# Kernel optimization log

Measured on AMD Instinct MI355X. Metric: run time of the kernel, lower is better.

Reference implementation:

```python
import jax, jax.numpy as jnp
import numpy as np

B, T, IN, H, FC, OUT = 512, 1024, 64, 128, 128, 1


def _glorot(key, shape, fan):
    bound = 1.0 / np.sqrt(fan)
    return jax.random.uniform(key, shape, jnp.float32, -bound, bound)


def setup_inputs() -> dict:
    key = jax.random.key(0)
    ks = jax.random.split(key, 16)
    inp = {"x": jax.random.normal(ks[0], (B, T, IN), jnp.float32)}
    # GRU layer 0 (input IN -> H), layer 1 (H -> H). PyTorch layout: [3H, in], [3H, H]
    inp["W_ih0"] = _glorot(ks[1], (3 * H, IN), H)
    inp["W_hh0"] = _glorot(ks[2], (3 * H, H), H)
    inp["b_ih0"] = _glorot(ks[3], (3 * H,), H)
    inp["b_hh0"] = _glorot(ks[4], (3 * H,), H)
    inp["W_ih1"] = _glorot(ks[5], (3 * H, H), H)
    inp["W_hh1"] = _glorot(ks[6], (3 * H, H), H)
    inp["b_ih1"] = _glorot(ks[7], (3 * H,), H)
    inp["b_hh1"] = _glorot(ks[8], (3 * H,), H)
    inp["fc1_w"] = _glorot(ks[9], (FC, H), H)
    inp["fc1_b"] = _glorot(ks[10], (FC,), H)
    inp["fc2_w"] = _glorot(ks[11], (OUT, FC), FC)
    inp["fc2_b"] = _glorot(ks[12], (OUT,), FC)
    return inp


def _gru_layer(x_seq, W_ih, W_hh, b_ih, b_hh):
    # x_seq: [T, B, in]. Precompute all input projections in one big GEMM.
    xg = jnp.einsum("tbi,gi->tbg", x_seq, W_ih) + b_ih  # [T, B, 3H]
    h0 = jnp.zeros((x_seq.shape[1], W_hh.shape[1]), x_seq.dtype)

    def step(h, xg_t):
        hg = h @ W_hh.T + b_hh  # [B, 3H]
        xr, xz, xn = jnp.split(xg_t, 3, axis=-1)
        hr, hz, hn = jnp.split(hg, 3, axis=-1)
        r = jax.nn.sigmoid(xr + hr)
        z = jax.nn.sigmoid(xz + hz)
        n = jnp.tanh(xn + r * hn)
        h_new = (1.0 - z) * n + z * h
        return h_new, h_new

    _, hs = jax.lax.scan(step, h0, xg)
    return hs  # [T, B, H]


def reference(x, W_ih0, W_hh0, b_ih0, b_hh0, W_ih1, W_hh1, b_ih1, b_hh1,
              fc1_w, fc1_b, fc2_w, fc2_b):
    xs = jnp.transpose(x, (1, 0, 2))  # [T, B, IN]
    h1 = _gru_layer(xs, W_ih0, W_hh0, b_ih0, b_hh0)  # dropout inactive (eval)
    h2 = _gru_layer(h1, W_ih1, W_hh1, b_ih1, b_hh1)
    last = h2[-1]  # [B, H] == gru_out[:, -1, :]
    y = jax.nn.relu(last @ fc1_w.T + fc1_b)
    return y @ fc2_w.T + fc2_b  # [B, OUT]
```

## Files before the change

### kernel.cpp

```cpp
#include <hip/hip_runtime.h>
#include <hip/hip_fp16.h>
#include <stdint.h>

#define TT   1024
#define NIN  64
#define HH   128
#define GG   384
#define RPB  2
#define NWG  256
#define NTHR 768

#define WB_IH0 0
#define WB_HH0 3072
#define WB_IH1 9216
#define WB_HH1 15360

typedef _Float16 half2v __attribute__((ext_vector_type(2)));

__device__ __forceinline__ float fdot2(uint32_t a, uint32_t b, float c) {
    return __builtin_amdgcn_fdot2(__builtin_bit_cast(half2v, a),
                                  __builtin_bit_cast(half2v, b), c, false);
}
__device__ __forceinline__ uint32_t pack2f(float a, float b) {
    half2v v; v[0] = (_Float16)a; v[1] = (_Float16)b;
    return __builtin_bit_cast(uint32_t, v);
}
__device__ __forceinline__ float sigm(float v)     { return 1.f / (1.f + __expf(-v)); }
__device__ __forceinline__ float tanhfast(float v) { return 2.f / (1.f + __expf(-2.f * v)) - 1.f; }

#define D4(A_, W_, S_) A_ = fdot2(W_.x, S_.x, A_); A_ = fdot2(W_.y, S_.y, A_); \
                       A_ = fdot2(W_.z, S_.z, A_); A_ = fdot2(W_.w, S_.w, A_);

#define PK8(M_, g_) M_(g_,0) M_(g_,1) M_(g_,2) M_(g_,3) M_(g_,4) M_(g_,5) M_(g_,6) M_(g_,7)
#define R8X(M_)     M_(0) M_(1) M_(2) M_(3) M_(4) M_(5) M_(6) M_(7)
#define DWDEF(g_,k_) uint4 W##g_##_##k_;
#define LW(g_,k_)    W##g_##_##k_ = wp[(g_)*wst + (k_)];
#define DG(g_,k_) D4(a##g_##_0, W##g_##_##k_, s0_) D4(a##g_##_1, W##g_##_##k_, s1_)
#define SK4(k_) { uint4 s0_ = pb0[k_], s1_ = pb1[k_]; DG(0,k_) DG(1,k_) DG(2,k_) DG(3,k_) }
#define SK3(k_) { uint4 s0_ = pb0[k_], s1_ = pb1[k_]; DG(0,k_) DG(1,k_) DG(2,k_) }

__global__ __launch_bounds__(256) void pack_weights(
    const float* __restrict__ Wih0, const float* __restrict__ Whh0,
    const float* __restrict__ Wih1, const float* __restrict__ Whh1,
    uint32_t* __restrict__ ws)
{
    const int i = blockIdx.x * 256 + threadIdx.x;
    const int P0 = 384 * 64 / 2, P1 = 384 * 128 / 2;
    const float* src; int off;
    if (i < P0)               { src = Wih0; off = i; }
    else if (i < P0 + P1)     { src = Whh0; off = i - P0; }
    else if (i < P0 + 2 * P1) { src = Wih1; off = i - P0 - P1; }
    else                      { src = Whh1; off = i - P0 - 2 * P1; }
    const float2 v = *(const float2*)(src + 2 * off);
    ws[i] = pack2f(v.x, v.y);
}

__global__ __launch_bounds__(NTHR)
__attribute__((amdgpu_waves_per_eu(3, 3)))
void gru_fused(
    const float* __restrict__ x,
    const uint32_t* __restrict__ wsw,
    const float* __restrict__ bih0, const float* __restrict__ bhh0,
    const float* __restrict__ bih1, const float* __restrict__ bhh1,
    const float* __restrict__ fc1w, const float* __restrict__ fc1b,
    const float* __restrict__ fc2w, const float* __restrict__ fc2b,
    float* __restrict__ out)
{
    __shared__ __align__(16) uint32_t xh[2][RPB][NIN / 2];
    __shared__ __align__(16) uint32_t h0h[RPB][HH / 2];
    __shared__ __align__(16) uint32_t h1h[RPB][HH / 2];
    __shared__ float h0f[RPB][HH];
    __shared__ float h1f[RPB][HH];
    __shared__ float pX0[RPB][GG];
    __shared__ __align__(16) float pH0q[RPB][96][2][4];
    __shared__ __align__(16) float pX1q[RPB][96][2][4];
    __shared__ __align__(16) float pH1q[RPB][96][2][4];

    const int lid  = threadIdx.x;
    const int row0 = blockIdx.x * RPB;

    PK8(DWDEF,0) PK8(DWDEF,1) PK8(DWDEF,2) PK8(DWDEF,3)
    float b0 = 0.f, b1 = 0.f, b2 = 0.f, b3 = 0.f;
    int gq_ = 0, kh_ = 0;
    const uint4 *pbA0 = nullptr, *pbA1 = nullptr;
    float2 xr2 = {0.f, 0.f};

    const uint4* wv = (const uint4*)wsw;

    if (lid < 128) {
        const int t = lid;
        const uint4* wp = wv + WB_IH0 + (3 * t) * 8; const int wst = 8;
        PK8(LW,0) PK8(LW,1) PK8(LW,2)
        b0 = bih0[3 * t]; b1 = bih0[3 * t + 1]; b2 = bih0[3 * t + 2];
    } else if (lid < 320) {
        const int t = lid - 128; gq_ = t >> 1; kh_ = t & 1;
        const uint4* wp = wv + WB_HH0 + (4 * gq_) * 16 + kh_ * 8; const int wst = 16;
        PK8(LW,0) PK8(LW,1) PK8(LW,2) PK8(LW,3)
        if (!kh_) { b0 = bhh0[4*gq_]; b1 = bhh0[4*gq_+1]; b2 = bhh0[4*gq_+2]; b3 = bhh0[4*gq_+3]; }
        pbA0 = (const uint4*)&h0h[0][0] + kh_ * 8;
        pbA1 = (const uint4*)&h0h[1][0] + kh_ * 8;
    } else if (lid < 512) {
        const int t = lid - 320; gq_ = t >> 1; kh_ = t & 1;
        const uint4* wp = wv + WB_IH1 + (4 * gq_) * 16 + kh_ * 8; const int wst = 16;
        PK8(LW,0) PK8(LW,1) PK8(LW,2) PK8(LW,3)
        if (!kh_) { b0 = bih1[4*gq_]; b1 = bih1[4*gq_+1]; b2 = bih1[4*gq_+2]; b3 = bih1[4*gq_+3]; }
        pbA0 = (const uint4*)&h0h[0][0] + kh_ * 8;
        pbA1 = (const uint4*)&h0h[1][0] + kh_ * 8;
    } else if (lid < 704) {
        const int t = lid - 512; gq_ = t >> 1; kh_ = t & 1;
        const uint4* wp = wv + WB_HH1 + (4 * gq_) * 16 + kh_ * 8; const int wst = 16;
        PK8(LW,0) PK8(LW,1) PK8(LW,2) PK8(LW,3)
        if (!kh_) { b0 = bhh1[4*gq_]; b1 = bhh1[4*gq_+1]; b2 = bhh1[4*gq_+2]; b3 = bhh1[4*gq_+3]; }
        pbA0 = (const uint4*)&h1h[0][0] + kh_ * 8;
        pbA1 = (const uint4*)&h1h[1][0] + kh_ * 8;
    } else {
        const int idx = lid - 704, r = idx >> 5, c = idx & 31;
        const float* xp = x + (size_t)(row0 + r) * TT * NIN + 2 * c;
        xh[0][r][c] = pack2f(xp[0], xp[1]);
        xr2 = *(const float2*)(xp + NIN);
    }

    if (lid < 128) {
        int r = lid >> 6, c = lid & 63;
        h0h[r][c] = 0u; h1h[r][c] = 0u;
    }
    if (lid < 256) {
        int r = lid >> 7, j = lid & 127;
        h0f[r][j] = 0.f; h1f[r][j] = 0.f;
    }
    __syncthreads();

    for (int i = 0; i <= TT; ++i) {
        if (lid < 128) {
            if (i < TT) {
                const uint4* pb0 = (const uint4*)&xh[i & 1][0][0];
                const uint4* pb1 = (const uint4*)&xh[i & 1][1][0];
                float a0_0 = b0, a0_1 = b0, a1_0 = b1, a1_1 = b1, a2_0 = b2, a2_1 = b2;
                R8X(SK3)
                const int g0 = 3 * lid;
                pX0[0][g0] = a0_0; pX0[0][g0+1] = a1_0; pX0[0][g0+2] = a2_0;
                pX0[1][g0] = a0_1; pX0[1][g0+1] = a1_1; pX0[1][g0+2] = a2_1;
            }
        } else if (lid < 320) {
            if (i < TT) {
                const uint4 *pb0 = pbA0, *pb1 = pbA1;
                float a0_0=b0,a0_1=b0,a1_0=b1,a1_1=b1,a2_0=b2,a2_1=b2,a3_0=b3,a3_1=b3;
                R8X(SK4)
                float4 v0 = {a0_0, a1_0, a2_0, a3_0};
                float4 v1 = {a0_1, a1_1, a2_1, a3_1};
                *(float4*)&pH0q[0][gq_][kh_][0] = v0;
                *(float4*)&pH0q[1][gq_][kh_][0] = v1;
            }
        } else if (lid < 512) {
            if (i >= 1) {
                const uint4 *pb0 = pbA0, *pb1 = pbA1;
                float a0_0=b0,a0_1=b0,a1_0=b1,a1_1=b1,a2_0=b2,a2_1=b2,a3_0=b3,a3_1=b3;
                R8X(SK4)
                float4 v0 = {a0_0, a1_0, a2_0, a3_0};
                float4 v1 = {a0_1, a1_1, a2_1, a3_1};
                *(float4*)&pX1q[0][gq_][kh_][0] = v0;
                *(float4*)&pX1q[1][gq_][kh_][0] = v1;
            }
        } else if (lid < 704) {
            if (i >= 1) {
                const uint4 *pb0 = pbA0, *pb1 = pbA1;
                float a0_0=b0,a0_1=b0,a1_0=b1,a1_1=b1,a2_0=b2,a2_1=b2,a3_0=b3,a3_1=b3;
                R8X(SK4)
                float4 v0 = {a0_0, a1_0, a2_0, a3_0};
                float4 v1 = {a0_1, a1_1, a2_1, a3_1};
                *(float4*)&pH1q[0][gq_][kh_][0] = v0;
                *(float4*)&pH1q[1][gq_][kh_][0] = v1;
            }
        } else {
            const int idx = lid - 704, r = idx >> 5, c = idx & 31;
            if (i + 1 < TT) xh[(i + 1) & 1][r][c] = pack2f(xr2.x, xr2.y);
            if (i + 2 < TT)
                xr2 = *(const float2*)(x + (size_t)(row0 + r) * TT * NIN
                                         + (size_t)(i + 2) * NIN + 2 * c);
        }
        __syncthreads();

        if (lid < 256) {
            if (i < TT) {
                const int r = lid >> 7, j = lid & 127;
                const int q = j >> 2, m = j & 3;
                float xr_ = pX0[r][j], xz_ = pX0[r][HH + j], xn_ = pX0[r][2*HH + j];
                float hr_ = pH0q[r][q][0][m]      + pH0q[r][q][1][m];
                float hz_ = pH0q[r][32 + q][0][m] + pH0q[r][32 + q][1][m];
                float hn_ = pH0q[r][64 + q][0][m] + pH0q[r][64 + q][1][m];
                float rg = sigm(xr_ + hr_);
                float zg = sigm(xz_ + hz_);
                float ng = tanhfast(fmaf(rg, hn_, xn_));
                float hnew = fmaf(zg, h0f[r][j] - ng, ng);
                h0f[r][j] = hnew;
                ((__half*)&h0h[r][0])[j] = __float2half(hnew);
            }
        } else if (lid < 512) {
            if (i >= 1) {
                const int t = lid - 256, r = t >> 7, j = t & 127;
                const int q = j >> 2, m = j & 3;
                float xr_ = pX1q[r][q][0][m]      + pX1q[r][q][1][m];
                float xz_ = pX1q[r][32 + q][0][m] + pX1q[r][32 + q][1][m];
                float xn_ = pX1q[r][64 + q][0][m] + pX1q[r][64 + q][1][m];
                float hr_ = pH1q[r][q][0][m]      + pH1q[r][q][1][m];
                float hz_ = pH1q[r][32 + q][0][m] + pH1q[r][32 + q][1][m];
                float hn_ = pH1q[r][64 + q][0][m] + pH1q[r][64 + q][1][m];
                float rg = sigm(xr_ + hr_);
                float zg = sigm(xz_ + hz_);
                float ng = tanhfast(fmaf(rg, hn_, xn_));
                float hnew = fmaf(zg, h1f[r][j] - ng, ng);
                h1f[r][j] = hnew;
                ((__half*)&h1h[r][0])[j] = __float2half(hnew);
            }
        }
        __syncthreads();
    }

    float yv = 0.f;
    if (lid < 256) {
        const int r = lid >> 7, j = lid & 127;
        const float* fr = fc1w + j * HH;
        float acc = fc1b[j];
        #pragma unroll 8
        for (int k = 0; k < HH; ++k) acc = fmaf(fr[k], h1f[r][k], acc);
        yv = fmaxf(acc, 0.f) * fc2w[j];
        #pragma unroll
        for (int m = 1; m < 64; m <<= 1) yv += __shfl_xor(yv, m, 64);
    }
    __syncthreads();
    if (lid < 256 && (lid & 63) == 0) pX0[0][lid >> 6] = yv;
    __syncthreads();
    if (lid < RPB) out[row0 + lid] = pX0[0][2 * lid] + pX0[0][2 * lid + 1] + fc2b[0];
}

extern "C" void kernel_launch(void* const* d_in, const int* in_sizes, int n_in,
                              void* d_out, int out_size, void* d_ws, size_t ws_size,
                              hipStream_t stream) {
    const float* x    = (const float*)d_in[0];
    const float* Wih0 = (const float*)d_in[1];
    const float* Whh0 = (const float*)d_in[2];
    const float* bih0 = (const float*)d_in[3];
    const float* bhh0 = (const float*)d_in[4];
    const float* Wih1 = (const float*)d_in[5];
    const float* Whh1 = (const float*)d_in[6];
    const float* bih1 = (const float*)d_in[7];
    const float* bhh1 = (const float*)d_in[8];
    const float* fc1w = (const float*)d_in[9];
    const float* fc1b = (const float*)d_in[10];
    const float* fc2w = (const float*)d_in[11];
    const float* fc2b = (const float*)d_in[12];

    uint32_t* ws = (uint32_t*)d_ws;

    pack_weights<<<dim3(86016 / 256), dim3(256), 0, stream>>>(Wih0, Whh0, Wih1, Whh1, ws);
    gru_fused<<<dim3(NWG), dim3(NTHR), 0, stream>>>(
        x, ws, bih0, bhh0, bih1, bhh1,
        fc1w, fc1b, fc2w, fc2b, (float*)d_out);
}
```

Baseline: 2.116 ms.

## Rebalance GRU work: six gates per thread, fewer waves, scheduled dot loop

```diff
diff --git a/kernel.cpp b/kernel.cpp
--- a/kernel.cpp
+++ b/kernel.cpp
@@ -5,10 +5,9 @@
 #define TT   1024
 #define NIN  64
 #define HH   128
-#define GG   384
 #define RPB  2
 #define NWG  256
-#define NTHR 768
+#define NTHR 512
 
 #define WB_IH0 0
 #define WB_HH0 3072
@@ -32,12 +31,18 @@
                        A_ = fdot2(W_.z, S_.z, A_); A_ = fdot2(W_.w, S_.w, A_);
 
 #define PK8(M_, g_) M_(g_,0) M_(g_,1) M_(g_,2) M_(g_,3) M_(g_,4) M_(g_,5) M_(g_,6) M_(g_,7)
+#define ALLW(M_)    PK8(M_,0) PK8(M_,1) PK8(M_,2) PK8(M_,3) PK8(M_,4) PK8(M_,5)
 #define R8X(M_)     M_(0) M_(1) M_(2) M_(3) M_(4) M_(5) M_(6) M_(7)
+
 #define DWDEF(g_,k_) uint4 W##g_##_##k_;
 #define LW(g_,k_)    W##g_##_##k_ = wp[(g_)*wst + (k_)];
-#define DG(g_,k_) D4(a##g_##_0, W##g_##_##k_, s0_) D4(a##g_##_1, W##g_##_##k_, s1_)
-#define SK4(k_) { uint4 s0_ = pb0[k_], s1_ = pb1[k_]; DG(0,k_) DG(1,k_) DG(2,k_) DG(3,k_) }
-#define SK3(k_) { uint4 s0_ = pb0[k_], s1_ = pb1[k_]; DG(0,k_) DG(1,k_) DG(2,k_) }
+#define PINW(g_,k_) asm volatile("" : "+v"(W##g_##_##k_.x), "+v"(W##g_##_##k_.y), \
+                                      "+v"(W##g_##_##k_.z), "+v"(W##g_##_##k_.w));
+#define PACE6 __builtin_amdgcn_sched_group_barrier(0x100, 2, 0); \
+              __builtin_amdgcn_sched_group_barrier(0x2, 48, 0);
+#define DG2(g_,k_) D4(ac##g_##_0, W##g_##_##k_, s0_) D4(ac##g_##_1, W##g_##_##k_, s1_)
+#define SK6(k_) { uint4 s0_ = pb0[k_], s1_ = pb1[k_]; \
+                  DG2(0,k_) DG2(1,k_) DG2(2,k_) DG2(3,k_) DG2(4,k_) DG2(5,k_) PACE6 }
 
 __global__ __launch_bounds__(256) void pack_weights(
     const float* __restrict__ Wih0, const float* __restrict__ Whh0,
@@ -56,7 +61,7 @@
 }
 
 __global__ __launch_bounds__(NTHR)
-__attribute__((amdgpu_waves_per_eu(3, 3)))
+__attribute__((amdgpu_waves_per_eu(2, 2)))
 void gru_fused(
     const float* __restrict__ x,
     const uint32_t* __restrict__ wsw,
@@ -71,55 +76,67 @@
     __shared__ __align__(16) uint32_t h1h[RPB][HH / 2];
     __shared__ float h0f[RPB][HH];
     __shared__ float h1f[RPB][HH];
-    __shared__ float pX0[RPB][GG];
-    __shared__ __align__(16) float pH0q[RPB][96][2][4];
-    __shared__ __align__(16) float pX1q[RPB][96][2][4];
-    __shared__ __align__(16) float pH1q[RPB][96][2][4];
+    __shared__ __align__(16) float pX0f[RPB * 6 * 64];
+    __shared__ __align__(16) float pH0qf[RPB * 2 * 6 * 64];
+    __shared__ __align__(16) float pX1qf[RPB * 2 * 6 * 64];
+    __shared__ __align__(16) float pH1qf[RPB * 2 * 6 * 64];
 
     const int lid  = threadIdx.x;
     const int row0 = blockIdx.x * RPB;
 
-    PK8(DWDEF,0) PK8(DWDEF,1) PK8(DWDEF,2) PK8(DWDEF,3)
-    float b0 = 0.f, b1 = 0.f, b2 = 0.f, b3 = 0.f;
-    int gq_ = 0, kh_ = 0;
-    const uint4 *pbA0 = nullptr, *pbA1 = nullptr;
+    ALLW(DWDEF)
+    float bb0 = 0.f, bb1 = 0.f, bb2 = 0.f, bb3 = 0.f, bb4 = 0.f, bb5 = 0.f;
+    int ilo = 0, ihi = TT;
+    const uint4 *pbS0 = nullptr, *pbS1 = nullptr;
+    float *wout0 = nullptr, *wout1 = nullptr;
     float2 xr2 = {0.f, 0.f};
 
     const uint4* wv = (const uint4*)wsw;
 
-    if (lid < 128) {
+    if (lid < 64) {
         const int t = lid;
-        const uint4* wp = wv + WB_IH0 + (3 * t) * 8; const int wst = 8;
-        PK8(LW,0) PK8(LW,1) PK8(LW,2)
-        b0 = bih0[3 * t]; b1 = bih0[3 * t + 1]; b2 = bih0[3 * t + 2];
+        const uint4* wp = wv + WB_IH0 + t * 8;  const int wst = 512;
+        ALLW(LW)
+        bb0=bih0[t]; bb1=bih0[t+64]; bb2=bih0[t+128]; bb3=bih0[t+192]; bb4=bih0[t+256]; bb5=bih0[t+320];
+        wout0 = &pX0f[t]; wout1 = &pX0f[384 + t];
+    } else if (lid < 192) {
+        const int t = (lid - 64) & 63, kh = (lid - 64) >> 6;
+        const uint4* wp = wv + WB_HH0 + t * 16 + kh * 8;  const int wst = 1024;
+        ALLW(LW)
+        if (!kh) { bb0=bhh0[t]; bb1=bhh0[t+64]; bb2=bhh0[t+128]; bb3=bhh0[t+192]; bb4=bhh0[t+256]; bb5=bhh0[t+320]; }
+        pbS0 = (const uint4*)&h0h[0][0] + kh * 8;
+        pbS1 = (const uint4*)&h0h[1][0] + kh * 8;
+        wout0 = &pH0qf[(kh * 6) * 64 + t];
+        wout1 = &pH0qf[((2 + kh) * 6) * 64 + t];
     } else if (lid < 320) {
-        const int t = lid - 128; gq_ = t >> 1; kh_ = t & 1;
-        const uint4* wp = wv + WB_HH0 + (4 * gq_) * 16 + kh_ * 8; const int wst = 16;
-        PK8(LW,0) PK8(LW,1) PK8(LW,2) PK8(LW,3)
-        if (!kh_) { b0 = bhh0[4*gq_]; b1 = bhh0[4*gq_+1]; b2 = bhh0[4*gq_+2]; b3 = bhh0[4*gq_+3]; }
-        pbA0 = (const uint4*)&h0h[0][0] + kh_ * 8;
-        pbA1 = (const uint4*)&h0h[1][0] + kh_ * 8;
-    } else if (lid < 512) {
-        const int t = lid - 320; gq_ = t >> 1; kh_ = t & 1;
-        const uint4* wp = wv + WB_IH1 + (4 * gq_) * 16 + kh_ * 8; const int wst = 16;
-        PK8(LW,0) PK8(LW,1) PK8(LW,2) PK8(LW,3)
-        if (!kh_) { b0 = bih1[4*gq_]; b1 = bih1[4*gq_+1]; b2 = bih1[4*gq_+2]; b3 = bih1[4*gq_+3]; }
-        pbA0 = (const uint4*)&h0h[0][0] + kh_ * 8;
-        pbA1 = (const uint4*)&h0h[1][0] + kh_ * 8;
-    } else if (lid < 704) {
-        const int t = lid - 512; gq_ = t >> 1; kh_ = t & 1;
-        const uint4* wp = wv + WB_HH1 + (4 * gq_) * 16 + kh_ * 8; const int wst = 16;
-        PK8(LW,0) PK8(LW,1) PK8(LW,2) PK8(LW,3)
-        if (!kh_) { b0 = bhh1[4*gq_]; b1 = bhh1[4*gq_+1]; b2 = bhh1[4*gq_+2]; b3 = bhh1[4*gq_+3]; }
-        pbA0 = (const uint4*)&h1h[0][0] + kh_ * 8;
-        pbA1 = (const uint4*)&h1h[1][0] + kh_ * 8;
+        const int t = (lid - 192) & 63, kh = (lid - 192) >> 6;
+        const uint4* wp = wv + WB_IH1 + t * 16 + kh * 8;  const int wst = 1024;
+        ALLW(LW)
+        if (!kh) { bb0=bih1[t]; bb1=bih1[t+64]; bb2=bih1[t+128]; bb3=bih1[t+192]; bb4=bih1[t+256]; bb5=bih1[t+320]; }
+        pbS0 = (const uint4*)&h0h[0][0] + kh * 8;
+        pbS1 = (const uint4*)&h0h[1][0] + kh * 8;
+        wout0 = &pX1qf[(kh * 6) * 64 + t];
+        wout1 = &pX1qf[((2 + kh) * 6) * 64 + t];
+        ilo = 1; ihi = TT + 1;
+    } else if (lid < 448) {
+        const int t = (lid - 320) & 63, kh = (lid - 320) >> 6;
+        const uint4* wp = wv + WB_HH1 + t * 16 + kh * 8;  const int wst = 1024;
+        ALLW(LW)
+        if (!kh) { bb0=bhh1[t]; bb1=bhh1[t+64]; bb2=bhh1[t+128]; bb3=bhh1[t+192]; bb4=bhh1[t+256]; bb5=bhh1[t+320]; }
+        pbS0 = (const uint4*)&h1h[0][0] + kh * 8;
+        pbS1 = (const uint4*)&h1h[1][0] + kh * 8;
+        wout0 = &pH1qf[(kh * 6) * 64 + t];
+        wout1 = &pH1qf[((2 + kh) * 6) * 64 + t];
+        ilo = 1; ihi = TT + 1;
     } else {
-        const int idx = lid - 704, r = idx >> 5, c = idx & 31;
+        const int idx = lid - 448, r = idx >> 5, c = idx & 31;
         const float* xp = x + (size_t)(row0 + r) * TT * NIN + 2 * c;
         xh[0][r][c] = pack2f(xp[0], xp[1]);
         xr2 = *(const float2*)(xp + NIN);
     }
 
+    if (lid < 448) { ALLW(PINW) }
+
     if (lid < 128) {
         int r = lid >> 6, c = lid & 63;
         h0h[r][c] = 0u; h1h[r][c] = 0u;
@@ -131,48 +148,22 @@
     __syncthreads();
 
     for (int i = 0; i <= TT; ++i) {
-        if (lid < 128) {
-            if (i < TT) {
-                const uint4* pb0 = (const uint4*)&xh[i & 1][0][0];
-                const uint4* pb1 = (const uint4*)&xh[i & 1][1][0];
-                float a0_0 = b0, a0_1 = b0, a1_0 = b1, a1_1 = b1, a2_0 = b2, a2_1 = b2;
-                R8X(SK3)
-                const int g0 = 3 * lid;
-                pX0[0][g0] = a0_0; pX0[0][g0+1] = a1_0; pX0[0][g0+2] = a2_0;
-                pX0[1][g0] = a0_1; pX0[1][g0+1] = a1_1; pX0[1][g0+2] = a2_1;
-            }
-        } else if (lid < 320) {
-            if (i < TT) {
-                const uint4 *pb0 = pbA0, *pb1 = pbA1;
-                float a0_0=b0,a0_1=b0,a1_0=b1,a1_1=b1,a2_0=b2,a2_1=b2,a3_0=b3,a3_1=b3;
-                R8X(SK4)
-                float4 v0 = {a0_0, a1_0, a2_0, a3_0};
-                float4 v1 = {a0_1, a1_1, a2_1, a3_1};
-                *(float4*)&pH0q[0][gq_][kh_][0] = v0;
-                *(float4*)&pH0q[1][gq_][kh_][0] = v1;
-            }
-        } else if (lid < 512) {
-            if (i >= 1) {
-                const uint4 *pb0 = pbA0, *pb1 = pbA1;
-                float a0_0=b0,a0_1=b0,a1_0=b1,a1_1=b1,a2_0=b2,a2_1=b2,a3_0=b3,a3_1=b3;
-                R8X(SK4)
-                float4 v0 = {a0_0, a1_0, a2_0, a3_0};
-                float4 v1 = {a0_1, a1_1, a2_1, a3_1};
-                *(float4*)&pX1q[0][gq_][kh_][0] = v0;
-                *(float4*)&pX1q[1][gq_][kh_][0] = v1;
-            }
-        } else if (lid < 704) {
-            if (i >= 1) {
-                const uint4 *pb0 = pbA0, *pb1 = pbA1;
-                float a0_0=b0,a0_1=b0,a1_0=b1,a1_1=b1,a2_0=b2,a2_1=b2,a3_0=b3,a3_1=b3;
-                R8X(SK4)
-                float4 v0 = {a0_0, a1_0, a2_0, a3_0};
-                float4 v1 = {a0_1, a1_1, a2_1, a3_1};
-                *(float4*)&pH1q[0][gq_][kh_][0] = v0;
-                *(float4*)&pH1q[1][gq_][kh_][0] = v1;
+        if (lid < 448) {
+            if (i >= ilo && i < ihi) {
+                const uint4* pb0 = pbS0;
+                const uint4* pb1 = pbS1;
+                if (lid < 64) {
+                    pb0 = (const uint4*)&xh[i & 1][0][0];
+                    pb1 = (const uint4*)&xh[i & 1][1][0];
+                }
+                float ac0_0=bb0, ac0_1=bb0, ac1_0=bb1, ac1_1=bb1, ac2_0=bb2, ac2_1=bb2,
+                      ac3_0=bb3, ac3_1=bb3, ac4_0=bb4, ac4_1=bb4, ac5_0=bb5, ac5_1=bb5;
+                R8X(SK6)
+                wout0[0]=ac0_0; wout0[64]=ac1_0; wout0[128]=ac2_0; wout0[192]=ac3_0; wout0[256]=ac4_0; wout0[320]=ac5_0;
+                wout1[0]=ac0_1; wout1[64]=ac1_1; wout1[128]=ac2_1; wout1[192]=ac3_1; wout1[256]=ac4_1; wout1[320]=ac5_1;
             }
         } else {
-            const int idx = lid - 704, r = idx >> 5, c = idx & 31;
+            const int idx = lid - 448, r = idx >> 5, c = idx & 31;
             if (i + 1 < TT) xh[(i + 1) & 1][r][c] = pack2f(xr2.x, xr2.y);
             if (i + 2 < TT)
                 xr2 = *(const float2*)(x + (size_t)(row0 + r) * TT * NIN
@@ -182,12 +173,13 @@
 
         if (lid < 256) {
             if (i < TT) {
-                const int r = lid >> 7, j = lid & 127;
-                const int q = j >> 2, m = j & 3;
-                float xr_ = pX0[r][j], xz_ = pX0[r][HH + j], xn_ = pX0[r][2*HH + j];
-                float hr_ = pH0q[r][q][0][m]      + pH0q[r][q][1][m];
-                float hz_ = pH0q[r][32 + q][0][m] + pH0q[r][32 + q][1][m];
-                float hn_ = pH0q[r][64 + q][0][m] + pH0q[r][64 + q][1][m];
+                const int r = lid >> 7, j = lid & 127, jh = j >> 6, jm = j & 63;
+                const float* pa = pX0f  + r * 384;
+                const float* ph = pH0qf + r * 768;
+                float xr_ = pa[jh*64 + jm], xz_ = pa[(2+jh)*64 + jm], xn_ = pa[(4+jh)*64 + jm];
+                float hr_ = ph[jh*64 + jm]     + ph[(6+jh)*64 + jm];
+                float hz_ = ph[(2+jh)*64 + jm] + ph[(8+jh)*64 + jm];
+                float hn_ = ph[(4+jh)*64 + jm] + ph[(10+jh)*64 + jm];
                 float rg = sigm(xr_ + hr_);
                 float zg = sigm(xz_ + hz_);
                 float ng = tanhfast(fmaf(rg, hn_, xn_));
@@ -195,16 +187,17 @@
                 h0f[r][j] = hnew;
                 ((__half*)&h0h[r][0])[j] = __float2half(hnew);
             }
-        } else if (lid < 512) {
+        } else {
             if (i >= 1) {
-                const int t = lid - 256, r = t >> 7, j = t & 127;
-                const int q = j >> 2, m = j & 3;
-                float xr_ = pX1q[r][q][0][m]      + pX1q[r][q][1][m];
-                float xz_ = pX1q[r][32 + q][0][m] + pX1q[r][32 + q][1][m];
-                float xn_ = pX1q[r][64 + q][0][m] + pX1q[r][64 + q][1][m];
-                float hr_ = pH1q[r][q][0][m]      + pH1q[r][q][1][m];
-                float hz_ = pH1q[r][32 + q][0][m] + pH1q[r][32 + q][1][m];
-                float hn_ = pH1q[r][64 + q][0][m] + pH1q[r][64 + q][1][m];
+                const int t = lid - 256, r = t >> 7, j = t & 127, jh = j >> 6, jm = j & 63;
+                const float* pa = pX1qf + r * 768;
+                const float* ph = pH1qf + r * 768;
+                float xr_ = pa[jh*64 + jm]     + pa[(6+jh)*64 + jm];
+                float xz_ = pa[(2+jh)*64 + jm] + pa[(8+jh)*64 + jm];
+                float xn_ = pa[(4+jh)*64 + jm] + pa[(10+jh)*64 + jm];
+                float hr_ = ph[jh*64 + jm]     + ph[(6+jh)*64 + jm];
+                float hz_ = ph[(2+jh)*64 + jm] + ph[(8+jh)*64 + jm];
+                float hn_ = ph[(4+jh)*64 + jm] + ph[(10+jh)*64 + jm];
                 float rg = sigm(xr_ + hr_);
                 float zg = sigm(xz_ + hz_);
                 float ng = tanhfast(fmaf(rg, hn_, xn_));
@@ -228,9 +221,9 @@
         for (int m = 1; m < 64; m <<= 1) yv += __shfl_xor(yv, m, 64);
     }
     __syncthreads();
-    if (lid < 256 && (lid & 63) == 0) pX0[0][lid >> 6] = yv;
+    if (lid < 256 && (lid & 63) == 0) pX0f[lid >> 6] = yv;
     __syncthreads();
-    if (lid < RPB) out[row0 + lid] = pX0[0][2 * lid] + pX0[0][2 * lid + 1] + fc2b[0];
+    if (lid < RPB) out[row0 + lid] = pX0f[2 * lid] + pX0f[2 * lid + 1] + fc2b[0];
 }
 
 extern "C" void kernel_launch(void* const* d_in, const int* in_sizes, int n_in,
```

New measurement: 2.216 ms. 1.05x slower.
